# Optimization experiments

Measured on AMD Instinct MI355X. Metric: run time of the kernel, lower is better.

Reference implementation:

```python
import jax, jax.numpy as jnp
import numpy as np

NM = 50000   # member nodes
NP = 50000   # provider nodes
DM = 96      # member feature dim
DP = 128     # provider feature dim
IN_DIM = 128
HID = 256
LAT = 64
E = 1000000


def _sage_conv(x, src, dst, n, Wl, Wr, b):
    # PyG SAGEConv, mean aggregation: out = lin_l(mean_j x_j) + lin_r(x)
    msg = x[src]                                           # [E2, F]
    agg = jax.ops.segment_sum(msg, dst, num_segments=n)    # [N, F]
    deg = jax.ops.segment_sum(jnp.ones(src.shape[0], x.dtype), dst, num_segments=n)
    agg = agg / jnp.maximum(deg, 1.0)[:, None]
    return agg @ Wl.T + b + x @ Wr.T


def setup_inputs() -> dict:
    key = jax.random.key(0)
    ks = jax.random.split(key, 12)
    def g(k, shape, scale):
        return jax.random.normal(k, shape, jnp.float32) * scale
    inp = {
        "x_member": jax.random.normal(ks[0], (NM, DM), jnp.float32),
        "x_provider": jax.random.normal(ks[1], (NP, DP), jnp.float32),
        "edge_index": jnp.stack([
            jax.random.randint(ks[2], (E,), 0, NP),   # provider idx
            jax.random.randint(ks[3], (E,), 0, NM),   # member idx
        ], axis=0),
        # SAGEConv 1
        "W1l": g(ks[4], (HID, IN_DIM), (1.0 / IN_DIM) ** 0.5),
        "W1r": g(ks[5], (HID, IN_DIM), (1.0 / IN_DIM) ** 0.5),
        "b1": jnp.zeros((HID,), jnp.float32),
        # SAGEConv 2
        "W2l": g(ks[6], (LAT, HID), (1.0 / HID) ** 0.5),
        "W2r": g(ks[7], (LAT, HID), (1.0 / HID) ** 0.5),
        "b2": jnp.zeros((LAT,), jnp.float32),
        # decoder Linear(latent, in_dim)
        "Wd": g(ks[8], (IN_DIM, LAT), (1.0 / LAT) ** 0.5),
        "bd": jnp.zeros((IN_DIM,), jnp.float32),
    }
    return inp


def reference(x_member, x_provider, edge_index, W1l, W1r, b1, W2l, W2r, b2, Wd, bd):
    # pad member features to max_dim and concat (members first)
    xm = jnp.pad(x_member, ((0, 0), (0, IN_DIM - DM)))
    x = jnp.concatenate([xm, x_provider], axis=0)          # [NM+NP, IN_DIM]

    provider_idx = edge_index[0]
    member_idx = edge_index[1]
    # faithful to source: member indices are offset by NM in the combined graph
    src = jnp.concatenate([provider_idx, member_idx + NM])
    dst = jnp.concatenate([member_idx + NM, provider_idx])
    n = NM + NP

    h = jax.nn.relu(_sage_conv(x, src, dst, n, W1l, W1r, b1))
    # dropout: eval mode -> identity
    z = _sage_conv(h, src, dst, n, W2l, W2r, b2)            # [N, LAT]
    x_hat = z @ Wd.T + bd                                   # [N, IN_DIM]

    x_hat_member = x_hat[:NM]
    x_hat_provider = x_hat[NM:]
    member_z = z[:NM]
    provider_z = z[NM:]
    edge_logits = jnp.sum(provider_z[provider_idx] * member_z[member_idx], axis=1)
    return (x_hat_member, x_hat_provider, edge_logits)
```

## Files before the change

kernel.cpp:

```cpp
#include <hip/hip_runtime.h>
#include <stdint.h>

#define NMEM 50000
#define NTOT 100000
#define DMEM 96
#define DPRV 128
#define IND  128
#define HID  256
#define LATD 64
#define NEDGE 1000000

#define NB   196
#define VSH  9
#define NBV  512
#define EPB  4096

typedef __bf16 v8bf  __attribute__((ext_vector_type(8)));
typedef float  f32x4 __attribute__((ext_vector_type(4)));

__device__ __forceinline__ float bf2f(uint32_t u) {
    union { uint32_t u; float f; } x; x.u = u << 16; return x.f;
}
__device__ __forceinline__ uint32_t f2bf(float f) {
    union { float f; uint32_t u; } x; x.f = f;
    uint32_t r = x.u + 0x7fffu + ((x.u >> 16) & 1u);
    return r >> 16;
}
__device__ __forceinline__ int ld_ei(const int* ei, int idx, int i64) {
    return i64 ? ei[2 * idx] : ei[idx];
}

__global__ void k_detect(const uint16_t* __restrict__ w1l, const int* __restrict__ ei,
                         int* __restrict__ flags) {
    __shared__ int c1, c2;
    if (threadIdx.x == 0) { c1 = 0; c2 = 0; }
    __syncthreads();
    int big = 0;
    for (int i = threadIdx.x; i < 32768; i += 256) {
        float w = bf2f(w1l[i]);
        if (!(w > -2.0f && w < 2.0f)) big++;
    }
    int zhi = 0;
    for (int j = threadIdx.x; j < 2048; j += 256)
        if (ei[2 * j + 1] == 0) zhi++;
    atomicAdd(&c1, big);
    atomicAdd(&c2, zhi);
    __syncthreads();
    if (threadIdx.x == 0) {
        flags[0] = (c1 > 64) ? 1 : 0;
        flags[1] = (c2 > 1024) ? 1 : 0;
    }
}

__global__ void k_canon(const void* w1l, const void* w1r, const void* w2l,
                        const void* w2r, const void* wd, const void* b1,
                        const void* b2, const void* bd,
                        uint16_t* __restrict__ dstw, float* __restrict__ dstb,
                        const int* __restrict__ flags) {
    int g = blockIdx.x * 256 + threadIdx.x;
    int f32in = flags[0];
    if (g < 106496) {
        const void* src; int off;
        if (g < 65536) { int n = g >> 8, k = g & 255;
            src = (k < 128) ? w1l : w1r; off = n * 128 + (k & 127); }
        else if (g < 81920) { src = w2l; off = g - 65536; }
        else if (g < 98304) { src = w2r; off = g - 81920; }
        else                { src = wd;  off = g - 98304; }
        dstw[g] = f32in ? (uint16_t)f2bf(((const float*)src)[off])
                        : ((const uint16_t*)src)[off];
    } else if (g < 106944) {
        int o = g - 106496;
        const void* src; int off;
        if (o < 256)      { src = b1; off = o; }
        else if (o < 320) { src = b2; off = o - 256; }
        else              { src = bd; off = o - 320; }
        dstb[o] = f32in ? ((const float*)src)[off] : bf2f(((const uint16_t*)src)[off]);
    }
}

__global__ void k_build_x(const void* xm, const void* xp, uint16_t* __restrict__ Px,
                          uint16_t* __restrict__ Rx, const int* __restrict__ flags) {
    int idx = blockIdx.x * 256 + threadIdx.x;
    if (idx >= NTOT * IND) return;
    int v = idx >> 7, d = idx & 127;
    int f32in = flags[0];
    uint16_t val;
    if (v < NMEM) {
        if (d < DMEM) {
            size_t o = (size_t)v * DMEM + d;
            val = f32in ? (uint16_t)f2bf(((const float*)xm)[o]) : ((const uint16_t*)xm)[o];
        } else val = 0;
    } else {
        size_t o = (size_t)(v - NMEM) * DPRV + d;
        val = f32in ? (uint16_t)f2bf(((const float*)xp)[o]) : ((const uint16_t*)xp)[o];
    }
    if (d < 64) Px[(size_t)v * 64 + d] = val;
    else        Rx[(size_t)v * 64 + (d - 64)] = val;
}

__global__ __launch_bounds__(256) void k_pcount(const int* __restrict__ ei,
                                                int* __restrict__ bcount,
                                                const int* __restrict__ flags) {
    __shared__ int h[NB];
    int t = threadIdx.x;
    for (int i = t; i < NB; i += 256) h[i] = 0;
    __syncthreads();
    int i64 = flags[1];
    int j0 = blockIdx.x * EPB;
    int jend = min(j0 + EPB, NEDGE);
    for (int j = j0 + t; j < jend; j += 256) {
        int p = ld_ei(ei, j, i64), m = ld_ei(ei, NEDGE + j, i64);
        atomicAdd(&h[(NMEM + m) >> VSH], 1);
        atomicAdd(&h[p >> VSH], 1);
    }
    __syncthreads();
    for (int i = t; i < NB; i += 256) atomicAdd(&bcount[i], h[i]);
}

__global__ void k_bscan(const int* __restrict__ bcount, int* __restrict__ bbase,
                        int* __restrict__ bcursor, int* __restrict__ row_start) {
    __shared__ int s[256];
    int t = threadIdx.x;
    int v = (t < NB) ? bcount[t] : 0;
    s[t] = v; __syncthreads();
    for (int off = 1; off < 256; off <<= 1) {
        int x = (t >= off) ? s[t - off] : 0;
        __syncthreads();
        s[t] += x;
        __syncthreads();
    }
    if (t < NB) { bbase[t] = s[t] - v; bcursor[t] = s[t] - v; }
    if (t == 0) { bbase[NB] = 2 * NEDGE; row_start[NTOT] = 2 * NEDGE; }
}

__global__ __launch_bounds__(256) void k_part(const int* __restrict__ ei,
                                              int* __restrict__ bcursor,
                                              uint32_t* __restrict__ part,
                                              const int* __restrict__ flags) {
    __shared__ int h[NB], gb[NB], cur[NB];
    int t = threadIdx.x;
    for (int i = t; i < NB; i += 256) { h[i] = 0; cur[i] = 0; }
    __syncthreads();
    int i64 = flags[1];
    int j0 = blockIdx.x * EPB;
    int jend = min(j0 + EPB, NEDGE);
    for (int j = j0 + t; j < jend; j += 256) {
        int p = ld_ei(ei, j, i64), m = ld_ei(ei, NEDGE + j, i64);
        atomicAdd(&h[(NMEM + m) >> VSH], 1);
        atomicAdd(&h[p >> VSH], 1);
    }
    __syncthreads();
    for (int i = t; i < NB; i += 256) gb[i] = atomicAdd(&bcursor[i], h[i]);
    __syncthreads();
    for (int j = j0 + t; j < jend; j += 256) {
        int p = ld_ei(ei, j, i64), m = ld_ei(ei, NEDGE + j, i64);
        int d1 = NMEM + m;
        int d2 = p;
        int b1 = d1 >> VSH, b2 = d2 >> VSH;
        int r1 = atomicAdd(&cur[b1], 1);
        part[gb[b1] + r1] = ((uint32_t)(d1 & (NBV - 1)) << 17) | (uint32_t)p;
        int r2 = atomicAdd(&cur[b2], 1);
        part[gb[b2] + r2] = ((uint32_t)(d2 & (NBV - 1)) << 17) | (uint32_t)(NMEM + m);
    }
}

__global__ __launch_bounds__(256) void k_sort(const uint32_t* __restrict__ part,
                                              const int* __restrict__ bbase,
                                              int* __restrict__ row_start,
                                              int* __restrict__ colg) {
    __shared__ int sa[NBV], sb[NBV];
    int k = blockIdx.x, t = threadIdx.x;
    int base = bbase[k];
    int cnt  = bbase[k + 1] - base;
    for (int i = t; i < NBV; i += 256) sa[i] = 0;
    __syncthreads();
    for (int i = t; i < cnt; i += 256) {
        uint32_t e = part[base + i];
        atomicAdd(&sa[e >> 17], 1);
    }
    __syncthreads();
    int* src = sa; int* dst = sb;
    for (int off = 1; off < NBV; off <<= 1) {
        for (int i = t; i < NBV; i += 256)
            dst[i] = src[i] + (i >= off ? src[i - off] : 0);
        __syncthreads();
        int* tmp = src; src = dst; dst = tmp;
    }
    for (int i = t; i < NBV; i += 256) {
        int excl = (i > 0) ? src[i - 1] : 0;
        dst[i] = excl;
        int gv = (k << VSH) + i;
        if (gv < NTOT) row_start[gv] = base + excl;
    }
    __syncthreads();
    for (int i = t; i < cnt; i += 256) {
        uint32_t e = part[base + i];
        int dloc = (int)(e >> 17);
        int pos = atomicAdd(&dst[dloc], 1);
        colg[base + pos] = (int)(e & 0x1FFFFu);
    }
}

__global__ __launch_bounds__(256) void k_agg1(const uint16_t* __restrict__ Px,
                                              const uint16_t* __restrict__ Rx,
                                              const int* __restrict__ row_start,
                                              const int* __restrict__ colg,
                                              uint16_t* __restrict__ A1) {
    int v = blockIdx.x * 4 + (threadIdx.x >> 6);
    int lane = threadIdx.x & 63;
    int slot = lane >> 4, cg = lane & 15;
    const uint16_t* base = (cg < 8) ? Px : Rx;
    int co = (cg & 7) * 8;
    int start = row_start[v], end = row_start[v + 1];
    float a[8] = {0.f, 0.f, 0.f, 0.f, 0.f, 0.f, 0.f, 0.f};
    for (int b = start + slot; b < end; b += 4) {
        int src = colg[b];
        union { uint4 q; uint16_t u[8]; } f;
        f.q = *(const uint4*)(base + (size_t)src * 64 + co);
#pragma unroll
        for (int i = 0; i < 8; i++) a[i] += bf2f(f.u[i]);
    }
#pragma unroll
    for (int i = 0; i < 8; i++) {
        a[i] += __shfl_xor(a[i], 16);
        a[i] += __shfl_xor(a[i], 32);
    }
    if (slot == 0) {
        float inv = 1.0f / (float)max(end - start, 1);
        union { uint4 q; uint16_t u[8]; } o;
#pragma unroll
        for (int i = 0; i < 8; i++) o.u[i] = (uint16_t)f2bf(a[i] * inv);
        *(uint4*)(A1 + (size_t)v * 128 + cg * 8) = o.q;
    }
}

__global__ __launch_bounds__(256, 2) void k_gemm1(const uint16_t* __restrict__ A1,
                                                  const uint16_t* __restrict__ canonb,
                                                  const float* __restrict__ biasf,
                                                  uint16_t* __restrict__ P,
                                                  uint16_t* __restrict__ R) {
    __shared__ uint16_t As[128][264];
    int t = threadIdx.x;
    int w = t >> 6, lane = t & 63;
    int m16 = lane & 15, q = lane >> 4;
    int row0 = blockIdx.x * 128;

    uint4 stg[16];
#pragma unroll
    for (int i = 0; i < 16; i++) {
        int c = t + i * 256;
        int row = c >> 5, seg = c & 31;
        int grow = min(row0 + row, NTOT - 1);
        int k0 = seg * 8;
        const uint16_t* src;
        if (k0 < 128)      src = A1 + (size_t)grow * 128 + k0;
        else if (k0 < 192) src = P + (size_t)grow * 64 + (k0 - 128);
        else               src = R + (size_t)grow * 64 + (k0 - 192);
        stg[i] = *(const uint4*)src;
    }
#pragma unroll
    for (int i = 0; i < 16; i++) {
        int c = t + i * 256;
        int row = c >> 5, seg = c & 31;
        *(uint4*)&As[row][seg * 8] = stg[i];
    }
    __syncthreads();

    uint32_t hpk[4][8][2];
#pragma unroll
    for (int p = 0; p < 2; p++) {
        v8bf b1[2][8];
#pragma unroll
        for (int n = 0; n < 2; n++) {
            int col = w * 64 + (p * 2 + n) * 16 + m16;
#pragma unroll
            for (int ks = 0; ks < 8; ks++)
                b1[n][ks] = *(const v8bf*)(canonb + (size_t)col * 256 + ks * 32 + q * 8);
        }
        f32x4 acc[8][2];
#pragma unroll
        for (int mt = 0; mt < 8; mt++) {
            acc[mt][0] = (f32x4){0.f, 0.f, 0.f, 0.f};
            acc[mt][1] = (f32x4){0.f, 0.f, 0.f, 0.f};
        }
#pragma unroll
        for (int mt = 0; mt < 8; mt++) {
#pragma unroll
            for (int ks = 0; ks < 8; ks++) {
                v8bf a = *(const v8bf*)&As[mt * 16 + m16][ks * 32 + q * 8];
                acc[mt][0] = __builtin_amdgcn_mfma_f32_16x16x32_bf16(b1[0][ks], a, acc[mt][0], 0, 0, 0);
                acc[mt][1] = __builtin_amdgcn_mfma_f32_16x16x32_bf16(b1[1][ks], a, acc[mt][1], 0, 0, 0);
            }
        }
#pragma unroll
        for (int n = 0; n < 2; n++) {
            int cb = w * 64 + (p * 2 + n) * 16 + q * 4;
            f32x4 bb = *(const f32x4*)&biasf[cb];
#pragma unroll
            for (int mt = 0; mt < 8; mt++) {
                float v0 = fmaxf(acc[mt][n][0] + bb[0], 0.f);
                float v1 = fmaxf(acc[mt][n][1] + bb[1], 0.f);
                float v2 = fmaxf(acc[mt][n][2] + bb[2], 0.f);
                float v3 = fmaxf(acc[mt][n][3] + bb[3], 0.f);
                hpk[p * 2 + n][mt][0] = f2bf(v0) | (f2bf(v1) << 16);
                hpk[p * 2 + n][mt][1] = f2bf(v2) | (f2bf(v3) << 16);
            }
        }
        if (p == 0) __builtin_amdgcn_sched_barrier(0);
    }
    __syncthreads();

#pragma unroll
    for (int pn = 0; pn < 4; pn++) {
        int cb = w * 64 + pn * 16 + q * 4;
#pragma unroll
        for (int mt = 0; mt < 8; mt++) {
            uint2 v; v.x = hpk[pn][mt][0]; v.y = hpk[pn][mt][1];
            *(uint2*)&As[mt * 16 + m16][cb] = v;
        }
    }
    __syncthreads();

    v8bf b2[2][8];
#pragma unroll
    for (int n = 0; n < 2; n++) {
        int c2 = w * 32 + n * 16 + m16;
        const uint16_t* s2 = canonb + (c2 < 64 ? (65536 + c2 * 256) : (81920 + (c2 - 64) * 256));
#pragma unroll
        for (int ks = 0; ks < 8; ks++)
            b2[n][ks] = *(const v8bf*)(s2 + ks * 32 + q * 8);
    }
    f32x4 acc2[8][2];
#pragma unroll
    for (int mt = 0; mt < 8; mt++) {
        acc2[mt][0] = (f32x4){0.f, 0.f, 0.f, 0.f};
        acc2[mt][1] = (f32x4){0.f, 0.f, 0.f, 0.f};
    }
#pragma unroll
    for (int mt = 0; mt < 8; mt++) {
#pragma unroll
        for (int ks = 0; ks < 8; ks++) {
            v8bf hf = *(const v8bf*)&As[mt * 16 + m16][ks * 32 + q * 8];
            acc2[mt][0] = __builtin_amdgcn_mfma_f32_16x16x32_bf16(b2[0][ks], hf, acc2[mt][0], 0, 0, 0);
            acc2[mt][1] = __builtin_amdgcn_mfma_f32_16x16x32_bf16(b2[1][ks], hf, acc2[mt][1], 0, 0, 0);
        }
    }
#pragma unroll
    for (int n = 0; n < 2; n++) {
        int cb = w * 32 + n * 16 + q * 4;
        int isR = cb >= 64;
        int cl = cb - (isR ? 64 : 0);
        f32x4 bb;
        if (isR) bb = *(const f32x4*)&biasf[256 + cl];
        else     bb = (f32x4){0.f, 0.f, 0.f, 0.f};
        uint16_t* dst = isR ? R : P;
#pragma unroll
        for (int mt = 0; mt < 8; mt++) {
            int row = row0 + mt * 16 + m16;
            if (row < NTOT) {
                uint2 v;
                v.x = f2bf(acc2[mt][n][0] + bb[0]) | (f2bf(acc2[mt][n][1] + bb[1]) << 16);
                v.y = f2bf(acc2[mt][n][2] + bb[2]) | (f2bf(acc2[mt][n][3] + bb[3]) << 16);
                *(uint2*)(dst + (size_t)row * 64 + cl) = v;
            }
        }
    }
}

__global__ __launch_bounds__(256) void k_agg2z(const uint16_t* __restrict__ P,
                                               const uint16_t* __restrict__ R,
                                               const int* __restrict__ row_start,
                                               const int* __restrict__ colg,
                                               uint16_t* __restrict__ Z) {
    int v = blockIdx.x * 4 + (threadIdx.x >> 6);
    int lane = threadIdx.x & 63;
    int slot = lane >> 3, cg = lane & 7;
    int start = row_start[v], end = row_start[v + 1];
    float a[8] = {0.f, 0.f, 0.f, 0.f, 0.f, 0.f, 0.f, 0.f};
    for (int b = start + slot; b < end; b += 8) {
        int src = colg[b];
        union { uint4 q; uint16_t u[8]; } f;
        f.q = *(const uint4*)(P + (size_t)src * 64 + cg * 8);
#pragma unroll
        for (int i = 0; i < 8; i++) a[i] += bf2f(f.u[i]);
    }
#pragma unroll
    for (int i = 0; i < 8; i++) {
        a[i] += __shfl_xor(a[i], 8);
        a[i] += __shfl_xor(a[i], 16);
        a[i] += __shfl_xor(a[i], 32);
    }
    if (slot == 0) {
        float inv = 1.0f / (float)max(end - start, 1);
        union { uint4 q; uint16_t u[8]; } rr, o;
        rr.q = *(const uint4*)(R + (size_t)v * 64 + cg * 8);
#pragma unroll
        for (int i = 0; i < 8; i++)
            o.u[i] = (uint16_t)f2bf(a[i] * inv + bf2f(rr.u[i]));
        *(uint4*)(Z + (size_t)v * 64 + cg * 8) = o.q;
    }
}

__global__ __launch_bounds__(256, 2) void k_gemm3(const uint16_t* __restrict__ Z,
                                                  const uint16_t* __restrict__ canonb,
                                                  const float* __restrict__ biasf,
                                                  float* __restrict__ outf) {
    int wave = threadIdx.x >> 6, lane = threadIdx.x & 63;
    int m16 = lane & 15, quad = lane >> 4;
    int row0 = (blockIdx.x * 4 + wave) * 16;
    int arow = min(row0 + m16, NTOT - 1);
    v8bf a0 = *(const v8bf*)(Z + (size_t)arow * 64 + quad * 8);
    v8bf a1 = *(const v8bf*)(Z + (size_t)arow * 64 + 32 + quad * 8);
    f32x4 acc[8];
#pragma unroll
    for (int i = 0; i < 8; i++) acc[i] = (f32x4){0.f, 0.f, 0.f, 0.f};
#pragma unroll
    for (int nt = 0; nt < 8; nt++) {
        v8bf b0 = *(const v8bf*)(canonb + 98304 + (size_t)(nt * 16 + m16) * 64 + quad * 8);
        v8bf b1 = *(const v8bf*)(canonb + 98304 + (size_t)(nt * 16 + m16) * 64 + 32 + quad * 8);
        acc[nt] = __builtin_amdgcn_mfma_f32_16x16x32_bf16(a0, b0, acc[nt], 0, 0, 0);
        acc[nt] = __builtin_amdgcn_mfma_f32_16x16x32_bf16(a1, b1, acc[nt], 0, 0, 0);
    }
#pragma unroll
    for (int nt = 0; nt < 8; nt++) {
        int col = nt * 16 + m16;
        float bia = biasf[320 + col];
#pragma unroll
        for (int r = 0; r < 4; r++) {
            int row = row0 + quad * 4 + r;
            if (row < NTOT) outf[(size_t)row * 128 + col] = acc[nt][r] + bia;
        }
    }
}

__global__ __launch_bounds__(256) void k_logits(const int* __restrict__ ei,
                                                const uint16_t* __restrict__ Z,
                                                float* __restrict__ out,
                                                const int* __restrict__ flags) {
    int t = blockIdx.x * 256 + threadIdx.x;
    int j = t >> 3, sub = t & 7;
    if (j >= NEDGE) return;
    int i64 = flags[1];
    int p = ld_ei(ei, j, i64), m = ld_ei(ei, NEDGE + j, i64);
    union { uint4 q; uint16_t u[8]; } a, b;
    a.q = *(const uint4*)(Z + (size_t)(NMEM + p) * 64 + sub * 8);
    b.q = *(const uint4*)(Z + (size_t)m * 64 + sub * 8);
    float d = 0.f;
#pragma unroll
    for (int i = 0; i < 8; i++) d += bf2f(a.u[i]) * bf2f(b.u[i]);
    d += __shfl_xor(d, 1);
    d += __shfl_xor(d, 2);
    d += __shfl_xor(d, 4);
    if (sub == 0) out[j] = d;
}

__global__ void k_zero_out(float* __restrict__ out, int n4) {
    int i = blockIdx.x * 256 + threadIdx.x;
    if (i < n4) ((uint4*)out)[i] = (uint4){0, 0, 0, 0};
}
__global__ void k_sentinel(float* __restrict__ out, const int* __restrict__ flags,
                           int ws_mb) {
    if (blockIdx.x == 0 && threadIdx.x == 0)
        out[0] = 1000.0f + (float)ws_mb + 4096.0f * flags[0] + 8192.0f * flags[1];
}

extern "C" void kernel_launch(void* const* d_in, const int* in_sizes, int n_in,
                              void* d_out, int out_size, void* d_ws, size_t ws_size,
                              hipStream_t stream) {
    const void* xm = d_in[0];
    const void* xp = d_in[1];
    const int*  ei = (const int*)d_in[2];
    float* outf = (float*)d_out;

    const size_t NEED = 73019648;
    if (ws_size < NEED) {
        int* flags = (int*)d_ws;
        k_detect<<<1, 256, 0, stream>>>((const uint16_t*)d_in[3], ei, flags);
        int n4 = out_size / 4;
        k_zero_out<<<(n4 + 255) / 256, 256, 0, stream>>>(outf, n4);
        k_sentinel<<<1, 64, 0, stream>>>(outf, flags, (int)(ws_size >> 20));
        return;
    }

    char* ws = (char*)d_ws;
    int* colg       = (int*)(ws + 0);
    int* bmeta      = (int*)(ws + 8000000);
    int* bucket_count  = bmeta;
    int* bucket_base   = bmeta + 256;
    int* bucket_cursor = bmeta + 512;
    int* row_start  = (int*)(ws + 8400384);
    int* flags      = (int*)(ws + 8800768) + 100;
    uint16_t* canonb= (uint16_t*)(ws + 8804864);
    float* biasf    = (float*)(ws + 9017856);
    uint16_t* A1    = (uint16_t*)(ws + 9019648);
    uint32_t* part  = (uint32_t*)A1;
    uint16_t* P     = (uint16_t*)(ws + 34619648);
    uint16_t* R     = (uint16_t*)(ws + 47419648);
    uint16_t* Z     = (uint16_t*)(ws + 60219648);

    const int PGRID = (NEDGE + EPB - 1) / EPB;

    k_detect<<<1, 256, 0, stream>>>((const uint16_t*)d_in[3], ei, flags);
    k_canon<<<418, 256, 0, stream>>>(d_in[3], d_in[4], d_in[6], d_in[7], d_in[9],
                                     d_in[5], d_in[8], d_in[10], canonb, biasf, flags);
    k_build_x<<<(NTOT * IND + 255) / 256, 256, 0, stream>>>(xm, xp, P, R, flags);
    hipMemsetAsync(bucket_count, 0, 256 * sizeof(int), stream);
    k_pcount<<<PGRID, 256, 0, stream>>>(ei, bucket_count, flags);
    k_bscan<<<1, 256, 0, stream>>>(bucket_count, bucket_base, bucket_cursor, row_start);
    k_part<<<PGRID, 256, 0, stream>>>(ei, bucket_cursor, part, flags);
    k_sort<<<NB, 256, 0, stream>>>(part, bucket_base, row_start, colg);
    k_agg1<<<NTOT / 4, 256, 0, stream>>>(P, R, row_start, colg, A1);
    k_gemm1<<<782, 256, 0, stream>>>(A1, canonb, biasf, P, R);
    k_agg2z<<<NTOT / 4, 256, 0, stream>>>(P, R, row_start, colg, Z);
    k_gemm3<<<1563, 256, 0, stream>>>(Z, canonb, biasf, outf);
    k_logits<<<NEDGE * 8 / 256, 256, 0, stream>>>(ei, Z, outf + 12800000, flags);
}
```

Measured before the change: 434.1 us.

## Vectorize input build, pack two nodes per wave in aggregations, hoist gemm3 B loads

k_build_x now handles 8 features per thread with 128-bit loads and stores instead of one element per thread. Both aggregation kernels now map two destination nodes to each 64-lane wave (32 lanes per node) and keep two independent accumulators, so each lane has two gathers in flight and fewer lanes sit idle on low-degree nodes. k_gemm3 loads all B fragments before the MFMA loop to hide load latency. These changes trade higher register use for better memory-level parallelism and fewer wasted lanes.

```diff
diff --git a/kernel.cpp b/kernel.cpp
--- a/kernel.cpp
+++ b/kernel.cpp
@@ -81,21 +81,47 @@
 __global__ void k_build_x(const void* xm, const void* xp, uint16_t* __restrict__ Px,
                           uint16_t* __restrict__ Rx, const int* __restrict__ flags) {
     int idx = blockIdx.x * 256 + threadIdx.x;
-    if (idx >= NTOT * IND) return;
-    int v = idx >> 7, d = idx & 127;
+    if (idx >= NTOT * 16) return;
+    int v = idx >> 4, dblk = idx & 15;
+    int d0 = dblk * 8;
     int f32in = flags[0];
-    uint16_t val;
+    union { uint4 q; uint16_t u[8]; } o;
     if (v < NMEM) {
-        if (d < DMEM) {
-            size_t o = (size_t)v * DMEM + d;
-            val = f32in ? (uint16_t)f2bf(((const float*)xm)[o]) : ((const uint16_t*)xm)[o];
-        } else val = 0;
+        if (d0 < DMEM) {
+            if (f32in) {
+                const float* s = (const float*)xm + (size_t)v * DMEM + d0;
+                uint4 lo = *(const uint4*)s;
+                uint4 hi = *(const uint4*)(s + 4);
+                const float* lf = (const float*)&lo;
+                const float* hf = (const float*)&hi;
+#pragma unroll
+                for (int i = 0; i < 4; i++) o.u[i] = (uint16_t)f2bf(lf[i]);
+#pragma unroll
+                for (int i = 0; i < 4; i++) o.u[4 + i] = (uint16_t)f2bf(hf[i]);
+            } else {
+                o.q = *(const uint4*)((const uint16_t*)xm + (size_t)v * DMEM + d0);
+            }
+        } else {
+            o.q = (uint4){0, 0, 0, 0};
+        }
     } else {
-        size_t o = (size_t)(v - NMEM) * DPRV + d;
-        val = f32in ? (uint16_t)f2bf(((const float*)xp)[o]) : ((const uint16_t*)xp)[o];
-    }
-    if (d < 64) Px[(size_t)v * 64 + d] = val;
-    else        Rx[(size_t)v * 64 + (d - 64)] = val;
+        int vv = v - NMEM;
+        if (f32in) {
+            const float* s = (const float*)xp + (size_t)vv * DPRV + d0;
+            uint4 lo = *(const uint4*)s;
+            uint4 hi = *(const uint4*)(s + 4);
+            const float* lf = (const float*)&lo;
+            const float* hf = (const float*)&hi;
+#pragma unroll
+            for (int i = 0; i < 4; i++) o.u[i] = (uint16_t)f2bf(lf[i]);
+#pragma unroll
+            for (int i = 0; i < 4; i++) o.u[4 + i] = (uint16_t)f2bf(hf[i]);
+        } else {
+            o.q = *(const uint4*)((const uint16_t*)xp + (size_t)vv * DPRV + d0);
+        }
+    }
+    if (d0 < 64) *(uint4*)(Px + (size_t)v * 64 + d0) = o.q;
+    else         *(uint4*)(Rx + (size_t)v * 64 + (d0 - 64)) = o.q;
 }
 
 __global__ __launch_bounds__(256) void k_pcount(const int* __restrict__ ei,
@@ -206,30 +232,42 @@
                                               const int* __restrict__ row_start,
                                               const int* __restrict__ colg,
                                               uint16_t* __restrict__ A1) {
-    int v = blockIdx.x * 4 + (threadIdx.x >> 6);
-    int lane = threadIdx.x & 63;
-    int slot = lane >> 4, cg = lane & 15;
+    int t = threadIdx.x;
+    int half = (t & 63) >> 5;
+    int v = blockIdx.x * 8 + (t >> 6) * 2 + half;
+    int l32 = t & 31;
+    int slot = l32 >> 4, cg = l32 & 15;
     const uint16_t* base = (cg < 8) ? Px : Rx;
     int co = (cg & 7) * 8;
     int start = row_start[v], end = row_start[v + 1];
-    float a[8] = {0.f, 0.f, 0.f, 0.f, 0.f, 0.f, 0.f, 0.f};
-    for (int b = start + slot; b < end; b += 4) {
-        int src = colg[b];
-        union { uint4 q; uint16_t u[8]; } f;
-        f.q = *(const uint4*)(base + (size_t)src * 64 + co);
-#pragma unroll
-        for (int i = 0; i < 8; i++) a[i] += bf2f(f.u[i]);
+    float a0[8] = {0.f, 0.f, 0.f, 0.f, 0.f, 0.f, 0.f, 0.f};
+    float a1[8] = {0.f, 0.f, 0.f, 0.f, 0.f, 0.f, 0.f, 0.f};
+    int b = start + slot;
+    for (; b + 2 < end; b += 4) {
+        int s0 = colg[b], s1 = colg[b + 2];
+        union { uint4 q; uint16_t u[8]; } f0, f1;
+        f0.q = *(const uint4*)(base + (size_t)s0 * 64 + co);
+        f1.q = *(const uint4*)(base + (size_t)s1 * 64 + co);
+#pragma unroll
+        for (int i = 0; i < 8; i++) { a0[i] += bf2f(f0.u[i]); a1[i] += bf2f(f1.u[i]); }
+    }
+    if (b < end) {
+        int s0 = colg[b];
+        union { uint4 q; uint16_t u[8]; } f0;
+        f0.q = *(const uint4*)(base + (size_t)s0 * 64 + co);
+#pragma unroll
+        for (int i = 0; i < 8; i++) a0[i] += bf2f(f0.u[i]);
     }
 #pragma unroll
     for (int i = 0; i < 8; i++) {
-        a[i] += __shfl_xor(a[i], 16);
-        a[i] += __shfl_xor(a[i], 32);
+        a0[i] += a1[i];
+        a0[i] += __shfl_xor(a0[i], 16);
     }
     if (slot == 0) {
         float inv = 1.0f / (float)max(end - start, 1);
         union { uint4 q; uint16_t u[8]; } o;
 #pragma unroll
-        for (int i = 0; i < 8; i++) o.u[i] = (uint16_t)f2bf(a[i] * inv);
+        for (int i = 0; i < 8; i++) o.u[i] = (uint16_t)f2bf(a0[i] * inv);
         *(uint4*)(A1 + (size_t)v * 128 + cg * 8) = o.q;
     }
 }
@@ -372,23 +410,35 @@
                                                const int* __restrict__ row_start,
                                                const int* __restrict__ colg,
                                                uint16_t* __restrict__ Z) {
-    int v = blockIdx.x * 4 + (threadIdx.x >> 6);
-    int lane = threadIdx.x & 63;
-    int slot = lane >> 3, cg = lane & 7;
+    int t = threadIdx.x;
+    int half = (t & 63) >> 5;
+    int v = blockIdx.x * 8 + (t >> 6) * 2 + half;
+    int l32 = t & 31;
+    int slot = l32 >> 3, cg = l32 & 7;
     int start = row_start[v], end = row_start[v + 1];
-    float a[8] = {0.f, 0.f, 0.f, 0.f, 0.f, 0.f, 0.f, 0.f};
-    for (int b = start + slot; b < end; b += 8) {
-        int src = colg[b];
-        union { uint4 q; uint16_t u[8]; } f;
-        f.q = *(const uint4*)(P + (size_t)src * 64 + cg * 8);
-#pragma unroll
-        for (int i = 0; i < 8; i++) a[i] += bf2f(f.u[i]);
+    float a0[8] = {0.f, 0.f, 0.f, 0.f, 0.f, 0.f, 0.f, 0.f};
+    float a1[8] = {0.f, 0.f, 0.f, 0.f, 0.f, 0.f, 0.f, 0.f};
+    int b = start + slot;
+    for (; b + 4 < end; b += 8) {
+        int s0 = colg[b], s1 = colg[b + 4];
+        union { uint4 q; uint16_t u[8]; } f0, f1;
+        f0.q = *(const uint4*)(P + (size_t)s0 * 64 + cg * 8);
+        f1.q = *(const uint4*)(P + (size_t)s1 * 64 + cg * 8);
+#pragma unroll
+        for (int i = 0; i < 8; i++) { a0[i] += bf2f(f0.u[i]); a1[i] += bf2f(f1.u[i]); }
+    }
+    if (b < end) {
+        int s0 = colg[b];
+        union { uint4 q; uint16_t u[8]; } f0;
+        f0.q = *(const uint4*)(P + (size_t)s0 * 64 + cg * 8);
+#pragma unroll
+        for (int i = 0; i < 8; i++) a0[i] += bf2f(f0.u[i]);
     }
 #pragma unroll
     for (int i = 0; i < 8; i++) {
-        a[i] += __shfl_xor(a[i], 8);
-        a[i] += __shfl_xor(a[i], 16);
-        a[i] += __shfl_xor(a[i], 32);
+        a0[i] += a1[i];
+        a0[i] += __shfl_xor(a0[i], 8);
+        a0[i] += __shfl_xor(a0[i], 16);
     }
     if (slot == 0) {
         float inv = 1.0f / (float)max(end - start, 1);
@@ -396,7 +446,7 @@
         rr.q = *(const uint4*)(R + (size_t)v * 64 + cg * 8);
 #pragma unroll
         for (int i = 0; i < 8; i++)
-            o.u[i] = (uint16_t)f2bf(a[i] * inv + bf2f(rr.u[i]));
+            o.u[i] = (uint16_t)f2bf(a0[i] * inv + bf2f(rr.u[i]));
         *(uint4*)(Z + (size_t)v * 64 + cg * 8) = o.q;
     }
 }
@@ -411,15 +461,19 @@
     int arow = min(row0 + m16, NTOT - 1);
     v8bf a0 = *(const v8bf*)(Z + (size_t)arow * 64 + quad * 8);
     v8bf a1 = *(const v8bf*)(Z + (size_t)arow * 64 + 32 + quad * 8);
+    v8bf b0[8], b1[8];
+#pragma unroll
+    for (int nt = 0; nt < 8; nt++) {
+        b0[nt] = *(const v8bf*)(canonb + 98304 + (size_t)(nt * 16 + m16) * 64 + quad * 8);
+        b1[nt] = *(const v8bf*)(canonb + 98304 + (size_t)(nt * 16 + m16) * 64 + 32 + quad * 8);
+    }
     f32x4 acc[8];
 #pragma unroll
     for (int i = 0; i < 8; i++) acc[i] = (f32x4){0.f, 0.f, 0.f, 0.f};
 #pragma unroll
     for (int nt = 0; nt < 8; nt++) {
-        v8bf b0 = *(const v8bf*)(canonb + 98304 + (size_t)(nt * 16 + m16) * 64 + quad * 8);
-        v8bf b1 = *(const v8bf*)(canonb + 98304 + (size_t)(nt * 16 + m16) * 64 + 32 + quad * 8);
-        acc[nt] = __builtin_amdgcn_mfma_f32_16x16x32_bf16(a0, b0, acc[nt], 0, 0, 0);
-        acc[nt] = __builtin_amdgcn_mfma_f32_16x16x32_bf16(a1, b1, acc[nt], 0, 0, 0);
+        acc[nt] = __builtin_amdgcn_mfma_f32_16x16x32_bf16(a0, b0[nt], acc[nt], 0, 0, 0);
+        acc[nt] = __builtin_amdgcn_mfma_f32_16x16x32_bf16(a1, b1[nt], acc[nt], 0, 0, 0);
     }
 #pragma unroll
     for (int nt = 0; nt < 8; nt++) {
@@ -503,15 +557,15 @@
     k_detect<<<1, 256, 0, stream>>>((const uint16_t*)d_in[3], ei, flags);
     k_canon<<<418, 256, 0, stream>>>(d_in[3], d_in[4], d_in[6], d_in[7], d_in[9],
                                      d_in[5], d_in[8], d_in[10], canonb, biasf, flags);
-    k_build_x<<<(NTOT * IND + 255) / 256, 256, 0, stream>>>(xm, xp, P, R, flags);
+    k_build_x<<<(NTOT * 16 + 255) / 256, 256, 0, stream>>>(xm, xp, P, R, flags);
     hipMemsetAsync(bucket_count, 0, 256 * sizeof(int), stream);
     k_pcount<<<PGRID, 256, 0, stream>>>(ei, bucket_count, flags);
     k_bscan<<<1, 256, 0, stream>>>(bucket_count, bucket_base, bucket_cursor, row_start);
     k_part<<<PGRID, 256, 0, stream>>>(ei, bucket_cursor, part, flags);
     k_sort<<<NB, 256, 0, stream>>>(part, bucket_base, row_start, colg);
-    k_agg1<<<NTOT / 4, 256, 0, stream>>>(P, R, row_start, colg, A1);
+    k_agg1<<<NTOT / 8, 256, 0, stream>>>(P, R, row_start, colg, A1);
     k_gemm1<<<782, 256, 0, stream>>>(A1, canonb, biasf, P, R);
-    k_agg2z<<<NTOT / 4, 256, 0, stream>>>(P, R, row_start, colg, Z);
+    k_agg2z<<<NTOT / 8, 256, 0, stream>>>(P, R, row_start, colg, Z);
     k_gemm3<<<1563, 256, 0, stream>>>(Z, canonb, biasf, outf);
     k_logits<<<NEDGE * 8 / 256, 256, 0, stream>>>(ei, Z, outf + 12800000, flags);
 }
```

Measured after the change: 394.6 us. 9.1% less time.
